# Kernel optimization log

Measured on AMD Instinct MI355X. Metric: run time of the kernel, lower is better.

The kernel has to match this reference:

```python
import jax, jax.numpy as jnp
import numpy as np

NUM_EXPERTS = 64
TOP_K = 2
CAPACITY_FACTOR = 1.25
D_MODEL = 2048
BATCH, SEQ = 4, 4096


def setup_inputs() -> dict:
    key = jax.random.key(0)
    kx, kw = jax.random.split(key)
    x = jax.random.normal(kx, (BATCH, SEQ, D_MODEL), dtype=jnp.float32)
    # router weight: Linear(input_dim, num_experts, bias=False), init std=0.001
    W = jax.random.normal(kw, (NUM_EXPERTS, D_MODEL), dtype=jnp.float32) * 0.001
    return {"x": x, "W": W}


def reference(x, W):
    B, S, D = x.shape
    N = B * S  # combined batch of tokens
    E = NUM_EXPERTS
    k = TOP_K
    capacity = int(CAPACITY_FACTOR * N * k / E)  # static Python int

    x_flat = x.reshape(N, D)
    router_logits = jnp.einsum('nd,ed->ne', x_flat, W)  # [N, E]
    routing_weights = jax.nn.softmax(router_logits, axis=-1)

    top_k_weights, top_k_indices = jax.lax.top_k(routing_weights, k)  # [N, k]
    top_k_weights = top_k_weights / (top_k_weights.sum(-1, keepdims=True) + 1e-8)

    expert_counts = jnp.zeros((E,), dtype=jnp.float32)
    dispatch_mask = jnp.zeros((N, E), dtype=jnp.float32)
    token_ids = jnp.arange(N)

    # Sequential over k (fixed, small): within a k-step the capacity check uses
    # counts from previous steps only, matching the torch scatter semantics.
    for k_idx in range(k):
        expert_idx = top_k_indices[:, k_idx]            # [N]
        under_cap = expert_counts[expert_idx] < capacity  # [N] bool
        expert_counts = expert_counts + jax.ops.segment_sum(
            under_cap.astype(jnp.float32), expert_idx, num_segments=E)
        # top-k experts are distinct per token, so add == set on zero-init slots
        dispatch_mask = dispatch_mask.at[token_ids, expert_idx].add(
            jnp.where(under_cap, top_k_weights[:, k_idx], 0.0))

    # Tokens that got dropped everywhere go to the least-loaded expert with w=1
    unrouted = dispatch_mask.sum(-1) == 0                     # [N]
    least_loaded = jnp.argmax(capacity - expert_counts)       # scalar
    dispatch_mask = jnp.where(
        unrouted[:, None] & (jnp.arange(E)[None, :] == least_loaded),
        1.0, dispatch_mask)

    normalized_dispatch_mask = dispatch_mask / (dispatch_mask.sum(-1, keepdims=True) + 1e-8)

    router_z_loss = jnp.mean(jnp.square(router_logits))
    counts = normalized_dispatch_mask.sum(0)                  # [E]
    target_count = float(N * k / E)
    load_balance_loss = jnp.mean(jnp.square(counts / float(N) - target_count / float(N)))
    router_loss = 0.001 * jax.lax.stop_gradient(router_z_loss) \
                + 0.001 * jax.lax.stop_gradient(load_balance_loss)

    return (jax.lax.stop_gradient(routing_weights), normalized_dispatch_mask, router_loss)
```

## Files before the change

kernel.cpp:

```cpp
#include <hip/hip_runtime.h>
#include <math.h>

#define N_TOK 16384
#define D_MODEL 2048
#define N_EXP 64
#define CAPACITY 640
#define NREP 8
#define NSTEP 64

typedef __attribute__((ext_vector_type(8))) _Float16 h8;
typedef __attribute__((ext_vector_type(4))) float f4;

#define AS1 __attribute__((address_space(1)))
#define AS3 __attribute__((address_space(3)))
__device__ __forceinline__ void gld16(const void* g, void* l) {
  __builtin_amdgcn_global_load_lds((const AS1 void*)g, (AS3 void*)l, 16, 0, 0);
}

__global__ __launch_bounds__(256) void k0_cvtw(const float* __restrict__ W,
                                               _Float16* __restrict__ WT) {
  const int lane = threadIdx.x & 63;
  const int c = blockIdx.x * 4 + (threadIdx.x >> 6);
  const int s = c >> 3, q = c & 7;
  const int part = q >> 2, nt = q & 3;
  const int e = nt * 16 + (lane & 15);
  const int k = s * 32 + (lane >> 4) * 8;
  const float* src = W + (size_t)e * D_MODEL + k;
  const float4 a = *(const float4*)src;
  const float4 b = *(const float4*)(src + 4);
  const float f[8] = {a.x, a.y, a.z, a.w, b.x, b.y, b.z, b.w};
  h8 out;
#pragma unroll
  for (int j = 0; j < 8; j++) {
    const float sc = f[j] * 1024.f;
    const _Float16 h = (_Float16)sc;
    out[j] = part ? (_Float16)((sc - (float)h) * 1024.f) : h;
  }
  *(h8*)(WT + (size_t)c * 512 + lane * 8) = out;
}

__global__ __launch_bounds__(128, 2) void k12_gemm_softmax(
    const float* __restrict__ x, const _Float16* __restrict__ WT,
    float* __restrict__ rw_out, int2* __restrict__ top12,
    float2* __restrict__ wts, int* __restrict__ histR,
    float* __restrict__ zR) {
  __shared__ __align__(16) float XR[2][3][512];
  __shared__ __align__(16) _Float16 WR[2][3][4096];

  const int t = threadIdx.x;
  const int lane = t & 63;
  const int w = t >> 6;
  const int m0w = blockIdx.x * 32 + w * 16;
  const int rep = blockIdx.x & (NREP - 1);

  const float* xb = x + (size_t)(m0w + (lane & 15)) * D_MODEL + (lane >> 4) * 8;
  const _Float16* wb = WT + lane * 8;

  f4 acc1[4], acc2[4];
#pragma unroll
  for (int i = 0; i < 4; i++) {
    acc1[i] = (f4)(0.f);
    acc2[i] = (f4)(0.f);
  }

#define STAGE(slot, s)                                            \
  {                                                               \
    gld16(xb + (s) * 32, &XR[w][slot][0]);                        \
    gld16(xb + (s) * 32 + 4, &XR[w][slot][256]);                  \
    _Pragma("unroll") for (int c = 0; c < 8; c++)                 \
        gld16(wb + (size_t)(s) * 4096 + c * 512, &WR[w][slot][c * 512]); \
  }
#define WAITV10 asm volatile("s_waitcnt vmcnt(10)" ::: "memory")
#define WAITV0 asm volatile("s_waitcnt vmcnt(0)" ::: "memory")

#define COMPUTE(slot)                                                       \
  {                                                                         \
    const f4 xa0 = *(const f4*)&XR[w][slot][lane * 4];                      \
    const f4 xa1 = *(const f4*)&XR[w][slot][256 + lane * 4];                \
    h8 ah, al;                                                              \
    const float xf[8] = {xa0[0], xa0[1], xa0[2], xa0[3],                    \
                         xa1[0], xa1[1], xa1[2], xa1[3]};                   \
    _Pragma("unroll") for (int j = 0; j < 8; j++) {                         \
      const _Float16 hv = (_Float16)xf[j];                                  \
      ah[j] = hv;                                                           \
      al[j] = (_Float16)((xf[j] - (float)hv) * 1024.f);                     \
    }                                                                       \
    _Pragma("unroll") for (int nt = 0; nt < 4; nt++) {                      \
      const h8 bh = *(const h8*)&WR[w][slot][nt * 512 + lane * 8];          \
      const h8 bl = *(const h8*)&WR[w][slot][(4 + nt) * 512 + lane * 8];    \
      acc1[nt] = __builtin_amdgcn_mfma_f32_16x16x32_f16(ah, bh, acc1[nt],   \
                                                        0, 0, 0);           \
      acc2[nt] = __builtin_amdgcn_mfma_f32_16x16x32_f16(al, bh, acc2[nt],   \
                                                        0, 0, 0);           \
      acc2[nt] = __builtin_amdgcn_mfma_f32_16x16x32_f16(ah, bl, acc2[nt],   \
                                                        0, 0, 0);           \
    }                                                                       \
  }

  STAGE(0, 0);
  STAGE(1, 1);
  for (int g = 0; g < 21; g++) {
    const int s = 3 * g;
    WAITV10;
    COMPUTE(0);
    STAGE(2, s + 2);
    WAITV10;
    COMPUTE(1);
    STAGE(0, s + 3);
    WAITV10;
    COMPUTE(2);
    if (g < 20) STAGE(1, s + 4);
  }
  WAITV0;
  COMPUTE(0);

  float* slog = (float*)&XR[w][0][0];
  const int cg = lane >> 4, ci = lane & 15;
#pragma unroll
  for (int nt = 0; nt < 4; nt++)
#pragma unroll
    for (int r = 0; r < 4; r++) {
      const float v =
          (acc1[nt][r] + acc2[nt][r] * 0.0009765625f) * 0.0009765625f;
      slog[(cg * 4 + r) * 65 + nt * 16 + ci] = v;
    }

  float z_acc = 0.f;
  for (int tt = 0; tt < 16; tt++) {
    const int n = m0w + tt;
    const float v = slog[tt * 65 + lane];
    z_acc += v * v;
    float mx = v;
#pragma unroll
    for (int off = 32; off; off >>= 1) mx = fmaxf(mx, __shfl_xor(mx, off));
    const float p = __expf(v - mx);
    float ssum = p;
#pragma unroll
    for (int off = 32; off; off >>= 1) ssum += __shfl_xor(ssum, off);
    const float rw = p / ssum;
    rw_out[(size_t)n * N_EXP + lane] = rw;

    const unsigned long long b1 = __ballot(v == mx);
    const int i1 = __builtin_ctzll(b1);
    float v2 = (lane == i1) ? -INFINITY : v;
#pragma unroll
    for (int off = 32; off; off >>= 1) v2 = fmaxf(v2, __shfl_xor(v2, off));
    const unsigned long long b2 = __ballot(v == v2) & ~(1ull << i1);
    const int i2 = __builtin_ctzll(b2);
    const float rw1 = __shfl(rw, i1);
    const float rw2 = __shfl(rw, i2);
    if (lane == 0) {
      const float denom = rw1 + rw2 + 1e-8f;
      top12[n] = make_int2(i1, i2);
      wts[n] = make_float2(rw1 / denom, rw2 / denom);
      atomicAdd(&histR[(rep * N_EXP + i1) * 16], 1);
    }
  }
#pragma unroll
  for (int off = 32; off; off >>= 1) z_acc += __shfl_xor(z_acc, off);
  if (lane == 0) atomicAdd(&zR[rep * 16], z_acc);
}

__global__ __launch_bounds__(256) void k3_dispatch(
    const int2* __restrict__ top12, const float2* __restrict__ wts,
    const int* __restrict__ histR, float* __restrict__ mask_out,
    float* __restrict__ cntR) {
  const int lane = threadIdx.x & 63;
  const int wid = threadIdx.x >> 6;
  const int n = blockIdx.x * 4 + wid;
  const int rep = blockIdx.x & (NREP - 1);

  const int2 ij = top12[n];
  const float2 w = wts[n];
  int h = 0;
#pragma unroll
  for (int r = 0; r < NREP; r++) h += histR[(r * N_EXP + ij.y) * 16];
  const bool allowed = h < CAPACITY;
  const float ssum = w.x + (allowed ? w.y : 0.f);
  const float inv = 1.f / (ssum + 1e-8f);
  float val = 0.f;
  if (lane == ij.x) val = w.x * inv;
  else if (allowed && lane == ij.y) val = w.y * inv;
  mask_out[(size_t)n * N_EXP + lane] = val;
  if (val != 0.f) atomicAdd(&cntR[(rep * N_EXP + lane) * 16], val);
}

__global__ void k4_loss(const float* __restrict__ cntR,
                        const float* __restrict__ zR,
                        float* __restrict__ loss_out) {
  const int lane = threadIdx.x;
  float c = 0.f;
#pragma unroll
  for (int r = 0; r < NREP; r++) c += cntR[(r * N_EXP + lane) * 16];
  const float d = (c - 512.0f) * (1.0f / 16384.0f);
  float v = d * d;
#pragma unroll
  for (int off = 32; off; off >>= 1) v += __shfl_xor(v, off);
  if (lane == 0) {
    float z = 0.f;
#pragma unroll
    for (int r = 0; r < NREP; r++) z += zR[r * 16];
    const float lb = v * (1.0f / 64.0f);
    loss_out[0] = 0.001f * (z * (1.0f / (16384.0f * 64.0f))) + 0.001f * lb;
  }
}

extern "C" void kernel_launch(void* const* d_in, const int* in_sizes, int n_in,
                              void* d_out, int out_size, void* d_ws,
                              size_t ws_size, hipStream_t stream) {
  const float* x = (const float*)d_in[0];
  const float* W = (const float*)d_in[1];
  float* out = (float*)d_out;
  float* rw_out = out;
  float* mask_out = out + (size_t)N_TOK * N_EXP;
  float* loss_out = out + 2 * (size_t)N_TOK * N_EXP;

  char* ws = (char*)d_ws;
  int* histR = (int*)ws;
  float* cntR = (float*)(ws + 32768);
  float* zR = (float*)(ws + 65536);
  int2* top12 = (int2*)(ws + 131072);
  float2* wts = (float2*)(ws + 262144);
  _Float16* WT = (_Float16*)(ws + 393216);

  hipMemsetAsync(histR, 0, 65536 + 512, stream);
  k0_cvtw<<<128, 256, 0, stream>>>(W, WT);
  k12_gemm_softmax<<<512, 128, 0, stream>>>(x, WT, rw_out, top12, wts, histR,
                                            zR);
  k3_dispatch<<<N_TOK / 4, 256, 0, stream>>>(top12, wts, histR, mask_out,
                                             cntR);
  k4_loss<<<1, 64, 0, stream>>>(cntR, zR, loss_out);
}
```

Measured before the change: 234.8 us.

## Split experts across waves, halve tokens per block, deepen load pipeline

Each block now covers 16 tokens instead of 32. Its two waves split the 64 experts in half, each wave staging only its own slice of the converted weights, and the grid doubles to 1024 blocks. The prefetch ring keeps three stages in flight instead of two, and the logits are combined through shared memory with block barriers before each wave runs softmax and top-2 on 8 tokens. The aim is more parallelism and more memory latency hidden per wave. The cost is that both waves load the same x rows, so x requests double unless L2 absorbs them, and two barriers are added.

```diff
diff --git a/kernel.cpp b/kernel.cpp
--- a/kernel.cpp
+++ b/kernel.cpp
@@ -44,39 +44,48 @@
     float* __restrict__ rw_out, int2* __restrict__ top12,
     float2* __restrict__ wts, int* __restrict__ histR,
     float* __restrict__ zR) {
-  __shared__ __align__(16) float XR[2][3][512];
-  __shared__ __align__(16) _Float16 WR[2][3][4096];
+  __shared__ __align__(16) char LB[36864];
 
   const int t = threadIdx.x;
   const int lane = t & 63;
   const int w = t >> 6;
-  const int m0w = blockIdx.x * 32 + w * 16;
+  const int m0 = blockIdx.x * 16;
   const int rep = blockIdx.x & (NREP - 1);
 
-  const float* xb = x + (size_t)(m0w + (lane & 15)) * D_MODEL + (lane >> 4) * 8;
+  char* ring = LB + w * 18432;
+#define XRs(slot) ((float*)(ring + (slot) * 6144))
+#define WRs(slot) ((_Float16*)(ring + (slot) * 6144 + 2048))
+
+  const float* xb = x + (size_t)(m0 + (lane & 15)) * D_MODEL + (lane >> 4) * 8;
   const _Float16* wb = WT + lane * 8;
 
-  f4 acc1[4], acc2[4];
-#pragma unroll
-  for (int i = 0; i < 4; i++) {
+  f4 acc1[2], acc2[2];
+#pragma unroll
+  for (int i = 0; i < 2; i++) {
     acc1[i] = (f4)(0.f);
     acc2[i] = (f4)(0.f);
   }
 
-#define STAGE(slot, s)                                            \
-  {                                                               \
-    gld16(xb + (s) * 32, &XR[w][slot][0]);                        \
-    gld16(xb + (s) * 32 + 4, &XR[w][slot][256]);                  \
-    _Pragma("unroll") for (int c = 0; c < 8; c++)                 \
-        gld16(wb + (size_t)(s) * 4096 + c * 512, &WR[w][slot][c * 512]); \
-  }
-#define WAITV10 asm volatile("s_waitcnt vmcnt(10)" ::: "memory")
+#define STAGE(slot, s)                                              \
+  {                                                                 \
+    gld16(xb + (s) * 32, XRs(slot));                                \
+    gld16(xb + (s) * 32 + 4, XRs(slot) + 256);                      \
+    gld16(wb + (size_t)(s) * 4096 + (2 * w + 0) * 512, WRs(slot));  \
+    gld16(wb + (size_t)(s) * 4096 + (2 * w + 1) * 512,              \
+          WRs(slot) + 512);                                         \
+    gld16(wb + (size_t)(s) * 4096 + (4 + 2 * w + 0) * 512,          \
+          WRs(slot) + 1024);                                        \
+    gld16(wb + (size_t)(s) * 4096 + (4 + 2 * w + 1) * 512,          \
+          WRs(slot) + 1536);                                        \
+  }
+#define WAITV12 asm volatile("s_waitcnt vmcnt(12)" ::: "memory")
+#define WAITV6 asm volatile("s_waitcnt vmcnt(6)" ::: "memory")
 #define WAITV0 asm volatile("s_waitcnt vmcnt(0)" ::: "memory")
 
 #define COMPUTE(slot)                                                       \
   {                                                                         \
-    const f4 xa0 = *(const f4*)&XR[w][slot][lane * 4];                      \
-    const f4 xa1 = *(const f4*)&XR[w][slot][256 + lane * 4];                \
+    const f4 xa0 = *(const f4*)&XRs(slot)[lane * 4];                        \
+    const f4 xa1 = *(const f4*)&XRs(slot)[256 + lane * 4];                  \
     h8 ah, al;                                                              \
     const float xf[8] = {xa0[0], xa0[1], xa0[2], xa0[3],                    \
                          xa1[0], xa1[1], xa1[2], xa1[3]};                   \
@@ -85,9 +94,9 @@
       ah[j] = hv;                                                           \
       al[j] = (_Float16)((xf[j] - (float)hv) * 1024.f);                     \
     }                                                                       \
-    _Pragma("unroll") for (int nt = 0; nt < 4; nt++) {                      \
-      const h8 bh = *(const h8*)&WR[w][slot][nt * 512 + lane * 8];          \
-      const h8 bl = *(const h8*)&WR[w][slot][(4 + nt) * 512 + lane * 8];    \
+    _Pragma("unroll") for (int nt = 0; nt < 2; nt++) {                      \
+      const h8 bh = *(const h8*)&WRs(slot)[nt * 512 + lane * 8];            \
+      const h8 bl = *(const h8*)&WRs(slot)[1024 + nt * 512 + lane * 8];     \
       acc1[nt] = __builtin_amdgcn_mfma_f32_16x16x32_f16(ah, bh, acc1[nt],   \
                                                         0, 0, 0);           \
       acc2[nt] = __builtin_amdgcn_mfma_f32_16x16x32_f16(al, bh, acc2[nt],   \
@@ -99,36 +108,47 @@
 
   STAGE(0, 0);
   STAGE(1, 1);
-  for (int g = 0; g < 21; g++) {
+  STAGE(2, 2);
+  for (int g = 0; g < 20; g++) {
     const int s = 3 * g;
-    WAITV10;
+    WAITV12;
     COMPUTE(0);
-    STAGE(2, s + 2);
-    WAITV10;
+    STAGE(0, s + 3);
+    WAITV12;
     COMPUTE(1);
-    STAGE(0, s + 3);
-    WAITV10;
+    STAGE(1, s + 4);
+    WAITV12;
     COMPUTE(2);
-    if (g < 20) STAGE(1, s + 4);
-  }
+    STAGE(2, s + 5);
+  }
+  WAITV12;
+  COMPUTE(0);
+  STAGE(0, 63);
+  WAITV12;
+  COMPUTE(1);
+  WAITV6;
+  COMPUTE(2);
   WAITV0;
   COMPUTE(0);
 
-  float* slog = (float*)&XR[w][0][0];
+  __syncthreads();
+  float* slog = (float*)LB;
   const int cg = lane >> 4, ci = lane & 15;
 #pragma unroll
-  for (int nt = 0; nt < 4; nt++)
+  for (int nt = 0; nt < 2; nt++)
 #pragma unroll
     for (int r = 0; r < 4; r++) {
       const float v =
           (acc1[nt][r] + acc2[nt][r] * 0.0009765625f) * 0.0009765625f;
-      slog[(cg * 4 + r) * 65 + nt * 16 + ci] = v;
+      slog[(cg * 4 + r) * 65 + (2 * w + nt) * 16 + ci] = v;
     }
+  __syncthreads();
 
   float z_acc = 0.f;
-  for (int tt = 0; tt < 16; tt++) {
-    const int n = m0w + tt;
-    const float v = slog[tt * 65 + lane];
+  for (int tt = 0; tt < 8; tt++) {
+    const int tloc = w * 8 + tt;
+    const int n = m0 + tloc;
+    const float v = slog[tloc * 65 + lane];
     z_acc += v * v;
     float mx = v;
 #pragma unroll
@@ -225,8 +245,8 @@
 
   hipMemsetAsync(histR, 0, 65536 + 512, stream);
   k0_cvtw<<<128, 256, 0, stream>>>(W, WT);
-  k12_gemm_softmax<<<512, 128, 0, stream>>>(x, WT, rw_out, top12, wts, histR,
-                                            zR);
+  k12_gemm_softmax<<<1024, 128, 0, stream>>>(x, WT, rw_out, top12, wts, histR,
+                                             zR);
   k3_dispatch<<<N_TOK / 4, 256, 0, stream>>>(top12, wts, histR, mask_out,
                                              cntR);
   k4_loss<<<1, 64, 0, stream>>>(cntR, zR, loss_out);
```

Result: slower. 239.8 us (+2.1%).

## Share router weight tiles across four waves with a four-slot barrier pipeline

Applied to the files above, without the earlier changes.

Before this, each wave loaded its own full copy of the fp16 weight tile into LDS. Now the GEMM block grows to 256 threads over 64 tokens, and the four waves split the weight-tile load and share it through LDS, which cuts redundant global weight traffic. The pipeline moves from three slots to four, using barriers and vmcnt waits so every wave sees the shared tiles before using them. In exchange there are per-step block barriers, launch bounds of one block, and a 64KB LDS footprint, which may lower occupancy and latency hiding.

```diff
diff --git a/kernel.cpp b/kernel.cpp
--- a/kernel.cpp
+++ b/kernel.cpp
@@ -39,19 +39,22 @@
   *(h8*)(WT + (size_t)c * 512 + lane * 8) = out;
 }
 
-__global__ __launch_bounds__(128, 2) void k12_gemm_softmax(
+__global__ __launch_bounds__(256, 1) void k12_gemm_softmax(
     const float* __restrict__ x, const _Float16* __restrict__ WT,
     float* __restrict__ rw_out, int2* __restrict__ top12,
     float2* __restrict__ wts, int* __restrict__ histR,
     float* __restrict__ zR) {
-  __shared__ __align__(16) float XR[2][3][512];
-  __shared__ __align__(16) _Float16 WR[2][3][4096];
+  __shared__ __align__(16) char LB[65536];
 
   const int t = threadIdx.x;
   const int lane = t & 63;
   const int w = t >> 6;
-  const int m0w = blockIdx.x * 32 + w * 16;
+  const int m0 = blockIdx.x * 64;
+  const int m0w = m0 + w * 16;
   const int rep = blockIdx.x & (NREP - 1);
+
+#define XSL(slot) ((float*)(LB + (slot) * 16384 + w * 2048))
+#define WSL(slot) ((_Float16*)(LB + (slot) * 16384 + 8192))
 
   const float* xb = x + (size_t)(m0w + (lane & 15)) * D_MODEL + (lane >> 4) * 8;
   const _Float16* wb = WT + lane * 8;
@@ -63,20 +66,24 @@
     acc2[i] = (f4)(0.f);
   }
 
-#define STAGE(slot, s)                                            \
-  {                                                               \
-    gld16(xb + (s) * 32, &XR[w][slot][0]);                        \
-    gld16(xb + (s) * 32 + 4, &XR[w][slot][256]);                  \
-    _Pragma("unroll") for (int c = 0; c < 8; c++)                 \
-        gld16(wb + (size_t)(s) * 4096 + c * 512, &WR[w][slot][c * 512]); \
-  }
-#define WAITV10 asm volatile("s_waitcnt vmcnt(10)" ::: "memory")
+#define STAGE(slot, s)                                                  \
+  {                                                                     \
+    gld16(xb + (s) * 32, XSL(slot));                                    \
+    gld16(xb + (s) * 32 + 4, XSL(slot) + 256);                          \
+    gld16(wb + (size_t)(s) * 4096 + (2 * w) * 512,                      \
+          WSL(slot) + (2 * w) * 512);                                   \
+    gld16(wb + (size_t)(s) * 4096 + (2 * w + 1) * 512,                  \
+          WSL(slot) + (2 * w + 1) * 512);                               \
+  }
+#define WAITV8 asm volatile("s_waitcnt vmcnt(8)" ::: "memory")
+#define WAITV4 asm volatile("s_waitcnt vmcnt(4)" ::: "memory")
 #define WAITV0 asm volatile("s_waitcnt vmcnt(0)" ::: "memory")
+#define BAR __builtin_amdgcn_s_barrier()
 
 #define COMPUTE(slot)                                                       \
   {                                                                         \
-    const f4 xa0 = *(const f4*)&XR[w][slot][lane * 4];                      \
-    const f4 xa1 = *(const f4*)&XR[w][slot][256 + lane * 4];                \
+    const f4 xa0 = *(const f4*)&XSL(slot)[lane * 4];                        \
+    const f4 xa1 = *(const f4*)&XSL(slot)[256 + lane * 4];                  \
     h8 ah, al;                                                              \
     const float xf[8] = {xa0[0], xa0[1], xa0[2], xa0[3],                    \
                          xa1[0], xa1[1], xa1[2], xa1[3]};                   \
@@ -86,8 +93,8 @@
       al[j] = (_Float16)((xf[j] - (float)hv) * 1024.f);                     \
     }                                                                       \
     _Pragma("unroll") for (int nt = 0; nt < 4; nt++) {                      \
-      const h8 bh = *(const h8*)&WR[w][slot][nt * 512 + lane * 8];          \
-      const h8 bl = *(const h8*)&WR[w][slot][(4 + nt) * 512 + lane * 8];    \
+      const h8 bh = *(const h8*)&WSL(slot)[nt * 512 + lane * 8];            \
+      const h8 bl = *(const h8*)&WSL(slot)[(4 + nt) * 512 + lane * 8];      \
       acc1[nt] = __builtin_amdgcn_mfma_f32_16x16x32_f16(ah, bh, acc1[nt],   \
                                                         0, 0, 0);           \
       acc2[nt] = __builtin_amdgcn_mfma_f32_16x16x32_f16(al, bh, acc2[nt],   \
@@ -96,25 +103,38 @@
                                                         0, 0, 0);           \
     }                                                                       \
   }
+#define STEP(slot, stslot, s) \
+  {                           \
+    WAITV8;                   \
+    BAR;                      \
+    STAGE(stslot, (s) + 3);   \
+    COMPUTE(slot);            \
+  }
 
   STAGE(0, 0);
   STAGE(1, 1);
-  for (int g = 0; g < 21; g++) {
-    const int s = 3 * g;
-    WAITV10;
-    COMPUTE(0);
-    STAGE(2, s + 2);
-    WAITV10;
-    COMPUTE(1);
-    STAGE(0, s + 3);
-    WAITV10;
-    COMPUTE(2);
-    if (g < 20) STAGE(1, s + 4);
-  }
+  STAGE(2, 2);
+  for (int g = 0; g < 15; g++) {
+    const int s = 4 * g;
+    STEP(0, 3, s);
+    STEP(1, 0, s + 1);
+    STEP(2, 1, s + 2);
+    STEP(3, 2, s + 3);
+  }
+  STEP(0, 3, 60);
+  WAITV8;
+  BAR;
+  COMPUTE(1);
+  WAITV4;
+  BAR;
+  COMPUTE(2);
   WAITV0;
-  COMPUTE(0);
-
-  float* slog = (float*)&XR[w][0][0];
+  BAR;
+  COMPUTE(3);
+
+  __syncthreads();
+
+  float* slog = (float*)(LB + w * 16384);
   const int cg = lane >> 4, ci = lane & 15;
 #pragma unroll
   for (int nt = 0; nt < 4; nt++)
@@ -225,8 +245,8 @@
 
   hipMemsetAsync(histR, 0, 65536 + 512, stream);
   k0_cvtw<<<128, 256, 0, stream>>>(W, WT);
-  k12_gemm_softmax<<<512, 128, 0, stream>>>(x, WT, rw_out, top12, wts, histR,
-                                            zR);
+  k12_gemm_softmax<<<N_TOK / 64, 256, 0, stream>>>(x, WT, rw_out, top12, wts,
+                                                   histR, zR);
   k3_dispatch<<<N_TOK / 4, 256, 0, stream>>>(top12, wts, histR, mask_out,
                                              cntR);
   k4_loss<<<1, 64, 0, stream>>>(cntR, zR, loss_out);
```

After: 221.5 us. -5.6%, faster.
